# Optimization experiments

Measured on AMD Instinct MI355X. Metric: run time of the kernel, lower is better.

Reference implementation:

```python
import jax, jax.numpy as jnp
import numpy as np

N_NODES = 50000
N_EDGES = 800000
IN_CH, HID, LAT = 256, 128, 64


def setup_inputs() -> dict:
    key = jax.random.key(0)
    k1, k2, k3, k4 = jax.random.split(key, 4)
    x = jax.random.normal(k1, (N_NODES, IN_CH), dtype=jnp.float32)
    edge_index = jax.random.randint(k2, (2, N_EDGES), 0, N_NODES, dtype=jnp.int64)
    W1 = jax.random.normal(k3, (IN_CH, HID), dtype=jnp.float32) * (1.0 / np.sqrt(IN_CH))
    b1 = jnp.zeros((HID,), dtype=jnp.float32)
    W2 = jax.random.normal(k4, (HID, LAT), dtype=jnp.float32) * (1.0 / np.sqrt(HID))
    b2 = jnp.zeros((LAT,), dtype=jnp.float32)
    return {"x": x, "edge_index": edge_index, "W1": W1, "b1": b1, "W2": W2, "b2": b2}


def gcn_conv(x, src, dst, deg_inv_sqrt, W, b):
    # PyG GCNConv: h = x @ W; out[dst] += d_dst^-1/2 * d_src^-1/2 * h[src]; + bias
    h = x @ W                                   # [N, out]
    norm = deg_inv_sqrt[src] * deg_inv_sqrt[dst]  # [E+N]
    msg = h[src] * norm[:, None]                # [E+N, out] (gather + scale)
    out = jax.ops.segment_sum(msg, dst, num_segments=x.shape[0])
    return out + b


def reference(x, edge_index, W1, b1, W2, b2):
    n = x.shape[0]
    loop = jnp.arange(n, dtype=edge_index.dtype)
    # add self loops (GCNConv default)
    src = jnp.concatenate([edge_index[0], loop])
    dst = jnp.concatenate([edge_index[1], loop])
    deg = jax.ops.segment_sum(jnp.ones_like(dst, dtype=x.dtype), dst, num_segments=n)
    deg_inv_sqrt = jnp.where(deg > 0, jax.lax.rsqrt(deg), 0.0)
    h = jax.nn.relu(gcn_conv(x, src, dst, deg_inv_sqrt, W1, b1))
    h = jax.nn.relu(gcn_conv(h, src, dst, deg_inv_sqrt, W2, b2))
    return h
```

## Files before the change

kernel.cpp:

```cpp
#include <hip/hip_runtime.h>

#define N_NODES 50000
#define N_EDGES 800000
#define IN_CH 256
#define HID 128
#define LAT 64
#define CAP 64
#define NBIN 196
#define BINCAP 4864

typedef __attribute__((ext_vector_type(8))) short short8;
typedef __attribute__((ext_vector_type(16))) float f32x16;

static __device__ __forceinline__ unsigned short bf16_rne(float x) {
    unsigned u = __float_as_uint(x);
    unsigned r = (u + 0x7FFFu + ((u >> 16) & 1u)) >> 16;
    return (unsigned short)r;
}
static __device__ __forceinline__ float bf16_to_f(unsigned short h) {
    return __uint_as_float(((unsigned)h) << 16);
}

static __device__ __forceinline__ void add8(uint4 p, float* a) {
    a[0] += __uint_as_float(p.x << 16);
    a[1] += __uint_as_float(p.x & 0xFFFF0000u);
    a[2] += __uint_as_float(p.y << 16);
    a[3] += __uint_as_float(p.y & 0xFFFF0000u);
    a[4] += __uint_as_float(p.z << 16);
    a[5] += __uint_as_float(p.z & 0xFFFF0000u);
    a[6] += __uint_as_float(p.w << 16);
    a[7] += __uint_as_float(p.w & 0xFFFF0000u);
}
static __device__ __forceinline__ void fma8(uint4 p, float m, float* a) {
    a[0] = fmaf(m, __uint_as_float(p.x << 16), a[0]);
    a[1] = fmaf(m, __uint_as_float(p.x & 0xFFFF0000u), a[1]);
    a[2] = fmaf(m, __uint_as_float(p.y << 16), a[2]);
    a[3] = fmaf(m, __uint_as_float(p.y & 0xFFFF0000u), a[3]);
    a[4] = fmaf(m, __uint_as_float(p.z << 16), a[4]);
    a[5] = fmaf(m, __uint_as_float(p.z & 0xFFFF0000u), a[5]);
    a[6] = fmaf(m, __uint_as_float(p.w << 16), a[6]);
    a[7] = fmaf(m, __uint_as_float(p.w & 0xFFFF0000u), a[7]);
}

template <int K, int NN>
static __device__ __forceinline__ void split_store(const float* __restrict__ W,
                                                   unsigned short* __restrict__ Wf, int i) {
    constexpr int CT = NN / 32;
    int k = i / NN, n = i % NN;
    float w = W[i];
    unsigned short hi = bf16_rne(w);
    unsigned short lo = bf16_rne(w - bf16_to_f(hi));
    size_t off = ((size_t)((k >> 4) * CT + (n >> 5)) * 64 + ((n & 31) + 32 * ((k >> 3) & 1))) * 8 + (k & 7);
    Wf[off] = hi;
    Wf[(size_t)K * NN + off] = lo;
}

__global__ __launch_bounds__(256) void prep_kernel(const float* __restrict__ W1,
                                                   const float* __restrict__ W2,
                                                   int* __restrict__ binCnt,
                                                   unsigned short* __restrict__ W1f,
                                                   unsigned short* __restrict__ W2f) {
    int i = blockIdx.x * blockDim.x + threadIdx.x;
    if (i < NBIN) binCnt[i] = 0;
    if (i < IN_CH * HID) split_store<IN_CH, HID>(W1, W1f, i);
    if (i < HID * LAT) split_store<HID, LAT>(W2, W2f, i);
}

__global__ __launch_bounds__(256) void fill1_kernel(const int* __restrict__ ei,
                                                    int* __restrict__ binCnt,
                                                    unsigned int* __restrict__ binBuf, int E) {
    __shared__ int hist[NBIN];
    __shared__ int base[NBIN];
    const int tid = threadIdx.x;
    for (int i = tid; i < NBIN; i += 256) hist[i] = 0;
    __syncthreads();

    const int e0 = blockIdx.x * 2048 + tid;
    unsigned int pk[8];
    int bn[8], ofs[8];
#pragma unroll
    for (int i = 0; i < 8; ++i) {
        int e = e0 + 256 * i;
        bool v = e < E;
        int s = v ? ei[e] : 0;
        int d = v ? ei[E + e] : 0;
        bn[i] = d >> 8;
        pk[i] = (unsigned int)s | ((unsigned int)(d & 255) << 16);
        ofs[i] = v ? atomicAdd(&hist[bn[i]], 1) : -1;
    }
    __syncthreads();
    for (int i = tid; i < NBIN; i += 256)
        base[i] = hist[i] ? atomicAdd(&binCnt[i], hist[i]) : 0;
    __syncthreads();
#pragma unroll
    for (int i = 0; i < 8; ++i) {
        if (ofs[i] >= 0) {
            int p = base[bn[i]] + ofs[i];
            if (p < BINCAP) binBuf[(size_t)bn[i] * BINCAP + p] = pk[i];
        }
    }
}

__global__ __launch_bounds__(256) void fill2_kernel(const int* __restrict__ binCnt,
                                                    const unsigned int* __restrict__ binBuf,
                                                    int* __restrict__ cnt,
                                                    unsigned short* __restrict__ colb) {
    __shared__ int lcnt[256];
    const int b = blockIdx.x;
    const int tid = threadIdx.x;
    lcnt[tid] = 0;
    __syncthreads();
    int n = binCnt[b]; if (n > BINCAP) n = BINCAP;
    const int node0 = b << 8;
    for (int i = tid; i < n; i += 256) {
        unsigned int pk = binBuf[(size_t)b * BINCAP + i];
        int local = pk >> 16;
        int s = pk & 0xFFFF;
        int slot = atomicAdd(&lcnt[local], 1);
        if (slot < CAP) colb[(size_t)(node0 + local) * CAP + slot] = (unsigned short)s;
    }
    __syncthreads();
    int node = node0 + tid;
    if (node < N_NODES) cnt[node] = lcnt[tid];
}

template <int K, int NN, bool AFP32>
__global__ __launch_bounds__(256) void gemm_kernel(const void* __restrict__ Av,
                                                   const unsigned short* __restrict__ Wf,
                                                   const int* __restrict__ cnt,
                                                   unsigned short* __restrict__ C, int M) {
    constexpr int CT = NN / 32;
    constexpr int MT = (NN == 128) ? 2 : 1;
    __shared__ unsigned short As[8 * 512];
    __shared__ unsigned short Bs[2 * 2 * CT * 512];

    const int tid = threadIdx.x;
    const int lane = tid & 63;
    const int w = tid >> 6;
    const int row0 = blockIdx.x * 128;
    const int rtb = (NN == 128) ? ((w >> 1) * 2) : w;
    const int ctb = (NN == 128) ? ((w & 1) * 2) : 0;

    f32x16 acc[MT][2];
#pragma unroll
    for (int mt = 0; mt < MT; ++mt)
#pragma unroll
        for (int nt = 0; nt < 2; ++nt)
#pragma unroll
            for (int q = 0; q < 16; ++q) acc[mt][nt][q] = 0.0f;

    for (int kt = 0; kt < K; kt += 32) {
        if constexpr (AFP32) {
            const float* A = (const float*)Av;
#pragma unroll
            for (int i = 0; i < 4; ++i) {
                int f = tid + 256 * i;
                int m = f >> 3, kq = f & 7;
                int row = row0 + m; if (row >= M) row = M - 1;
                const float4 v = *(const float4*)(A + (size_t)row * K + kt + kq * 4);
                ushort4 hi4 = make_ushort4(bf16_rne(v.x), bf16_rne(v.y), bf16_rne(v.z), bf16_rne(v.w));
                int k0 = kq * 4;
                int s = k0 >> 4, half = (k0 >> 3) & 1, j0 = k0 & 7, t = m >> 5;
                int ln = (m & 31) + 32 * half;
                *(ushort4*)&As[((s * 4 + t) << 9) + (ln << 3) + j0] = hi4;
            }
        } else {
            const unsigned short* A = (const unsigned short*)Av;
#pragma unroll
            for (int i = 0; i < 2; ++i) {
                int f = tid + 256 * i;
                int m = f >> 2, kc = f & 3;
                int row = row0 + m; if (row >= M) row = M - 1;
                uint4 v = *(const uint4*)(A + (size_t)row * K + kt + kc * 8);
                int s = kc >> 1, half = kc & 1, t = m >> 5;
                int ln = (m & 31) + 32 * half;
                *(uint4*)&As[((s * 4 + t) << 9) + (ln << 3)] = v;
            }
        }
        {
            const int sg0 = kt >> 4;
#pragma unroll
            for (int p = 0; p < 2; ++p)
#pragma unroll
                for (int sl = 0; sl < 2; ++sl) {
                    const float4* src = (const float4*)(Wf + (size_t)p * K * NN + (size_t)(sg0 + sl) * CT * 512);
                    float4* dst = (float4*)(Bs + (((p * 2 + sl) * CT) << 9));
                    for (int c0 = w * 64; c0 < CT * 64; c0 += 256) {
                        __builtin_amdgcn_global_load_lds(
                            (const __attribute__((address_space(1))) unsigned int*)(src + c0 + lane),
                            (__attribute__((address_space(3))) unsigned int*)(dst + c0),
                            16, 0, 0);
                    }
                }
        }
        __syncthreads();

#pragma unroll
        for (int sl = 0; sl < 2; ++sl) {
            short8 a[MT], bh[2], bl[2];
#pragma unroll
            for (int mt = 0; mt < MT; ++mt)
                a[mt] = *(const short8*)&As[((sl * 4 + rtb + mt) << 9) + (lane << 3)];
#pragma unroll
            for (int nt = 0; nt < 2; ++nt) {
                bh[nt] = *(const short8*)&Bs[((sl * CT + ctb + nt) << 9) + (lane << 3)];
                bl[nt] = *(const short8*)&Bs[(((2 + sl) * CT + ctb + nt) << 9) + (lane << 3)];
            }
#pragma unroll
            for (int mt = 0; mt < MT; ++mt)
#pragma unroll
                for (int nt = 0; nt < 2; ++nt) {
                    acc[mt][nt] = __builtin_amdgcn_mfma_f32_32x32x16_bf16(a[mt], bh[nt], acc[mt][nt], 0, 0, 0);
                    acc[mt][nt] = __builtin_amdgcn_mfma_f32_32x32x16_bf16(a[mt], bl[nt], acc[mt][nt], 0, 0, 0);
                }
        }
        __syncthreads();
    }

#pragma unroll
    for (int mt = 0; mt < MT; ++mt) {
#pragma unroll
        for (int r = 0; r < 16; ++r) {
            int rowl = (rtb + mt) * 32 + (r & 3) + 8 * (r >> 2) + 4 * (lane >> 5);
            int row = row0 + rowl;
            if (row < M) {
                float sc = rsqrtf((float)cnt[row] + 1.0f);
#pragma unroll
                for (int nt = 0; nt < 2; ++nt) {
                    int col = (ctb + nt) * 32 + (lane & 31);
                    C[(size_t)row * NN + col] = bf16_rne(acc[mt][nt][r] * sc);
                }
            }
        }
    }
}

template <int C, bool OBF16>
__global__ __launch_bounds__(256) void agg_kernel(const int* __restrict__ cnt,
                                                  const unsigned short* __restrict__ colb,
                                                  const unsigned short* __restrict__ hs,
                                                  const float* __restrict__ bias,
                                                  void* __restrict__ outv, int N) {
    constexpr int LPN = C / 8;
    constexpr int NPW = 64 / LPN;
    int node = (int)((blockIdx.x * blockDim.x + threadIdx.x) >> 6);
    int lane = threadIdx.x & 63;
    if (node >= N) return;
    const int g = lane / LPN;
    const int c = lane % LPN;

    int deg = cnt[node];
    int kk = deg < CAP ? deg : CAP;

    float acc[8];
#pragma unroll
    for (int q = 0; q < 8; ++q) acc[q] = 0.0f;
    if (g == 0) add8(*(const uint4*)(hs + (size_t)node * C + c * 8), acc);

    int myc = (lane < kk) ? (int)colb[(size_t)node * CAP + lane] : 0;

    int j = 0;
    for (; j + NPW * 4 <= kk; j += NPW * 4) {
        int s0 = __shfl(myc, j + g);
        int s1 = __shfl(myc, j + g + NPW);
        int s2 = __shfl(myc, j + g + 2 * NPW);
        int s3 = __shfl(myc, j + g + 3 * NPW);
        uint4 p0 = *(const uint4*)(hs + (size_t)s0 * C + c * 8);
        uint4 p1 = *(const uint4*)(hs + (size_t)s1 * C + c * 8);
        uint4 p2 = *(const uint4*)(hs + (size_t)s2 * C + c * 8);
        uint4 p3 = *(const uint4*)(hs + (size_t)s3 * C + c * 8);
        add8(p0, acc); add8(p1, acc); add8(p2, acc); add8(p3, acc);
    }
    if (j < kk) {
        bool v0 = (j + g) < kk, v1 = (j + g + NPW) < kk,
             v2 = (j + g + 2 * NPW) < kk, v3 = (j + g + 3 * NPW) < kk;
        int s0 = __shfl(myc, v0 ? (j + g) : 0);
        int s1 = __shfl(myc, v1 ? (j + g + NPW) : 0);
        int s2 = __shfl(myc, v2 ? (j + g + 2 * NPW) : 0);
        int s3 = __shfl(myc, v3 ? (j + g + 3 * NPW) : 0);
        uint4 p0 = *(const uint4*)(hs + (size_t)s0 * C + c * 8);
        uint4 p1 = *(const uint4*)(hs + (size_t)s1 * C + c * 8);
        uint4 p2 = *(const uint4*)(hs + (size_t)s2 * C + c * 8);
        uint4 p3 = *(const uint4*)(hs + (size_t)s3 * C + c * 8);
        fma8(p0, v0 ? 1.0f : 0.0f, acc);
        fma8(p1, v1 ? 1.0f : 0.0f, acc);
        fma8(p2, v2 ? 1.0f : 0.0f, acc);
        fma8(p3, v3 ? 1.0f : 0.0f, acc);
    }

#pragma unroll
    for (int s = LPN; s < 64; s <<= 1)
#pragma unroll
        for (int q = 0; q < 8; ++q) acc[q] += __shfl_xor(acc[q], s);

    if (lane < LPN) {
        float di = rsqrtf((float)deg + 1.0f);
        float o[8];
#pragma unroll
        for (int q = 0; q < 8; ++q)
            o[q] = fmaxf(fmaf(di, acc[q], bias[c * 8 + q]), 0.0f);
        if constexpr (OBF16) {
            unsigned short* out = (unsigned short*)outv;
            ushort4 lo4 = make_ushort4(bf16_rne(o[0]), bf16_rne(o[1]), bf16_rne(o[2]), bf16_rne(o[3]));
            ushort4 hi4 = make_ushort4(bf16_rne(o[4]), bf16_rne(o[5]), bf16_rne(o[6]), bf16_rne(o[7]));
            *(ushort4*)(out + (size_t)node * C + c * 8) = lo4;
            *(ushort4*)(out + (size_t)node * C + c * 8 + 4) = hi4;
        } else {
            float* out = (float*)outv;
            float4 o0 = {o[0], o[1], o[2], o[3]};
            float4 o1 = {o[4], o[5], o[6], o[7]};
            *(float4*)(out + (size_t)node * C + c * 8) = o0;
            *(float4*)(out + (size_t)node * C + c * 8 + 4) = o1;
        }
    }
}

extern "C" void kernel_launch(void* const* d_in, const int* in_sizes, int n_in,
                              void* d_out, int out_size, void* d_ws, size_t ws_size,
                              hipStream_t stream) {
    const float* x  = (const float*)d_in[0];
    const int*   ei = (const int*)d_in[1];
    const float* W1 = (const float*)d_in[2];
    const float* b1 = (const float*)d_in[3];
    const float* W2 = (const float*)d_in[4];
    const float* b2 = (const float*)d_in[5];

    const int N = N_NODES, E = N_EDGES;

    char* ws = (char*)d_ws;
    size_t off = 0;
    auto alloc = [&](size_t bytes) {
        void* p = ws + off;
        off = (off + bytes + 255) & ~(size_t)255;
        return p;
    };
    int*            cnt    = (int*)alloc((size_t)N * 4);
    unsigned short* colb   = (unsigned short*)alloc((size_t)N * CAP * 2);
    int*            binCnt = (int*)alloc((size_t)NBIN * 4);
    unsigned int*   binBuf = (unsigned int*)alloc((size_t)NBIN * BINCAP * 4);
    unsigned short* W1f    = (unsigned short*)alloc((size_t)2 * IN_CH * HID * 2);
    unsigned short* W2f    = (unsigned short*)alloc((size_t)2 * HID * LAT * 2);
    unsigned short* h1s    = (unsigned short*)alloc((size_t)N * HID * 2);
    unsigned short* act1   = (unsigned short*)alloc((size_t)N * HID * 2);
    unsigned short* h2s    = h1s;

    prep_kernel<<<(N + 255) / 256, 256, 0, stream>>>(W1, W2, binCnt, W1f, W2f);
    fill1_kernel<<<(E + 2047) / 2048, 256, 0, stream>>>(ei, binCnt, binBuf, E);
    fill2_kernel<<<NBIN, 256, 0, stream>>>(binCnt, binBuf, cnt, colb);

    gemm_kernel<IN_CH, HID, true><<<(N + 127) / 128, 256, 0, stream>>>(x, W1f, cnt, h1s, N);
    agg_kernel<HID, true><<<(N + 3) / 4, 256, 0, stream>>>(cnt, colb, h1s, b1, act1, N);

    gemm_kernel<HID, LAT, false><<<(N + 127) / 128, 256, 0, stream>>>(act1, W2f, cnt, h2s, N);
    agg_kernel<LAT, false><<<(N + 3) / 4, 256, 0, stream>>>(cnt, colb, h2s, b2, d_out, N);
}
```

Before: 213.6 us.

## Halve GEMM row tile to 64 and stage weights via plain vector loads

```diff
diff --git a/kernel.cpp b/kernel.cpp
--- a/kernel.cpp
+++ b/kernel.cpp
@@ -130,106 +130,85 @@
                                                    const int* __restrict__ cnt,
                                                    unsigned short* __restrict__ C, int M) {
     constexpr int CT = NN / 32;
-    constexpr int MT = (NN == 128) ? 2 : 1;
-    __shared__ unsigned short As[8 * 512];
+    constexpr int NT = (NN == 128) ? 2 : 1;
+    __shared__ unsigned short As[4 * 512];
     __shared__ unsigned short Bs[2 * 2 * CT * 512];
 
     const int tid = threadIdx.x;
     const int lane = tid & 63;
     const int w = tid >> 6;
-    const int row0 = blockIdx.x * 128;
-    const int rtb = (NN == 128) ? ((w >> 1) * 2) : w;
-    const int ctb = (NN == 128) ? ((w & 1) * 2) : 0;
-
-    f32x16 acc[MT][2];
-#pragma unroll
-    for (int mt = 0; mt < MT; ++mt)
-#pragma unroll
-        for (int nt = 0; nt < 2; ++nt)
-#pragma unroll
-            for (int q = 0; q < 16; ++q) acc[mt][nt][q] = 0.0f;
+    const int row0 = blockIdx.x * 64;
+    const int rt = w >> 1;
+    const int ct0 = (NN == 128) ? ((w & 1) * 2) : (w & 1);
+
+    f32x16 acc[NT];
+#pragma unroll
+    for (int nt = 0; nt < NT; ++nt)
+#pragma unroll
+        for (int q = 0; q < 16; ++q) acc[nt][q] = 0.0f;
 
     for (int kt = 0; kt < K; kt += 32) {
-        if constexpr (AFP32) {
-            const float* A = (const float*)Av;
-#pragma unroll
-            for (int i = 0; i < 4; ++i) {
-                int f = tid + 256 * i;
-                int m = f >> 3, kq = f & 7;
-                int row = row0 + m; if (row >= M) row = M - 1;
-                const float4 v = *(const float4*)(A + (size_t)row * K + kt + kq * 4);
-                ushort4 hi4 = make_ushort4(bf16_rne(v.x), bf16_rne(v.y), bf16_rne(v.z), bf16_rne(v.w));
-                int k0 = kq * 4;
-                int s = k0 >> 4, half = (k0 >> 3) & 1, j0 = k0 & 7, t = m >> 5;
-                int ln = (m & 31) + 32 * half;
-                *(ushort4*)&As[((s * 4 + t) << 9) + (ln << 3) + j0] = hi4;
-            }
-        } else {
-            const unsigned short* A = (const unsigned short*)Av;
-#pragma unroll
-            for (int i = 0; i < 2; ++i) {
-                int f = tid + 256 * i;
-                int m = f >> 2, kc = f & 3;
-                int row = row0 + m; if (row >= M) row = M - 1;
-                uint4 v = *(const uint4*)(A + (size_t)row * K + kt + kc * 8);
-                int s = kc >> 1, half = kc & 1, t = m >> 5;
-                int ln = (m & 31) + 32 * half;
-                *(uint4*)&As[((s * 4 + t) << 9) + (ln << 3)] = v;
-            }
+        {
+            int m = tid >> 2, kc = tid & 3;
+            int row = row0 + m; if (row >= M) row = M - 1;
+            int s = kc >> 1, half = kc & 1, t = m >> 5;
+            int ln = (m & 31) + 32 * half;
+            uint4 v;
+            if constexpr (AFP32) {
+                const float* A = (const float*)Av;
+                const float4 v0 = *(const float4*)(A + (size_t)row * K + kt + kc * 8);
+                const float4 v1 = *(const float4*)(A + (size_t)row * K + kt + kc * 8 + 4);
+                v.x = (unsigned)bf16_rne(v0.x) | ((unsigned)bf16_rne(v0.y) << 16);
+                v.y = (unsigned)bf16_rne(v0.z) | ((unsigned)bf16_rne(v0.w) << 16);
+                v.z = (unsigned)bf16_rne(v1.x) | ((unsigned)bf16_rne(v1.y) << 16);
+                v.w = (unsigned)bf16_rne(v1.z) | ((unsigned)bf16_rne(v1.w) << 16);
+            } else {
+                const unsigned short* A = (const unsigned short*)Av;
+                v = *(const uint4*)(A + (size_t)row * K + kt + kc * 8);
+            }
+            *(uint4*)&As[((s * 2 + t) << 9) + (ln << 3)] = v;
         }
         {
             const int sg0 = kt >> 4;
 #pragma unroll
-            for (int p = 0; p < 2; ++p)
-#pragma unroll
-                for (int sl = 0; sl < 2; ++sl) {
-                    const float4* src = (const float4*)(Wf + (size_t)p * K * NN + (size_t)(sg0 + sl) * CT * 512);
-                    float4* dst = (float4*)(Bs + (((p * 2 + sl) * CT) << 9));
-                    for (int c0 = w * 64; c0 < CT * 64; c0 += 256) {
-                        __builtin_amdgcn_global_load_lds(
-                            (const __attribute__((address_space(1))) unsigned int*)(src + c0 + lane),
-                            (__attribute__((address_space(3))) unsigned int*)(dst + c0),
-                            16, 0, 0);
-                    }
-                }
+            for (int i0 = 0; i0 < CT * 256; i0 += 256) {
+                int i = i0 + tid;
+                int psl = i / (CT * 64), rem = i % (CT * 64);
+                int p = psl >> 1, sl = psl & 1;
+                const uint4* src = (const uint4*)(Wf + (size_t)p * K * NN + (size_t)(sg0 + sl) * CT * 512);
+                ((uint4*)Bs)[i] = src[rem];
+            }
         }
         __syncthreads();
 
 #pragma unroll
         for (int sl = 0; sl < 2; ++sl) {
-            short8 a[MT], bh[2], bl[2];
-#pragma unroll
-            for (int mt = 0; mt < MT; ++mt)
-                a[mt] = *(const short8*)&As[((sl * 4 + rtb + mt) << 9) + (lane << 3)];
-#pragma unroll
-            for (int nt = 0; nt < 2; ++nt) {
-                bh[nt] = *(const short8*)&Bs[((sl * CT + ctb + nt) << 9) + (lane << 3)];
-                bl[nt] = *(const short8*)&Bs[(((2 + sl) * CT + ctb + nt) << 9) + (lane << 3)];
-            }
-#pragma unroll
-            for (int mt = 0; mt < MT; ++mt)
-#pragma unroll
-                for (int nt = 0; nt < 2; ++nt) {
-                    acc[mt][nt] = __builtin_amdgcn_mfma_f32_32x32x16_bf16(a[mt], bh[nt], acc[mt][nt], 0, 0, 0);
-                    acc[mt][nt] = __builtin_amdgcn_mfma_f32_32x32x16_bf16(a[mt], bl[nt], acc[mt][nt], 0, 0, 0);
-                }
+            short8 a = *(const short8*)&As[((sl * 2 + rt) << 9) + (lane << 3)];
+            short8 bh[NT], bl[NT];
+#pragma unroll
+            for (int nt = 0; nt < NT; ++nt) {
+                bh[nt] = *(const short8*)&Bs[((sl * CT + ct0 + nt) << 9) + (lane << 3)];
+                bl[nt] = *(const short8*)&Bs[(((2 + sl) * CT + ct0 + nt) << 9) + (lane << 3)];
+            }
+#pragma unroll
+            for (int nt = 0; nt < NT; ++nt) {
+                acc[nt] = __builtin_amdgcn_mfma_f32_32x32x16_bf16(a, bh[nt], acc[nt], 0, 0, 0);
+                acc[nt] = __builtin_amdgcn_mfma_f32_32x32x16_bf16(a, bl[nt], acc[nt], 0, 0, 0);
+            }
         }
         __syncthreads();
     }
 
 #pragma unroll
-    for (int mt = 0; mt < MT; ++mt) {
-#pragma unroll
-        for (int r = 0; r < 16; ++r) {
-            int rowl = (rtb + mt) * 32 + (r & 3) + 8 * (r >> 2) + 4 * (lane >> 5);
-            int row = row0 + rowl;
-            if (row < M) {
-                float sc = rsqrtf((float)cnt[row] + 1.0f);
-#pragma unroll
-                for (int nt = 0; nt < 2; ++nt) {
-                    int col = (ctb + nt) * 32 + (lane & 31);
-                    C[(size_t)row * NN + col] = bf16_rne(acc[mt][nt][r] * sc);
-                }
+    for (int r = 0; r < 16; ++r) {
+        int rowl = rt * 32 + (r & 3) + 8 * (r >> 2) + 4 * (lane >> 5);
+        int row = row0 + rowl;
+        if (row < M) {
+            float sc = rsqrtf((float)cnt[row] + 1.0f);
+#pragma unroll
+            for (int nt = 0; nt < NT; ++nt) {
+                int col = (ct0 + nt) * 32 + (lane & 31);
+                C[(size_t)row * NN + col] = bf16_rne(acc[nt][r] * sc);
             }
         }
     }
@@ -348,9 +327,9 @@
     fill1_kernel<<<(E + 2047) / 2048, 256, 0, stream>>>(ei, binCnt, binBuf, E);
     fill2_kernel<<<NBIN, 256, 0, stream>>>(binCnt, binBuf, cnt, colb);
 
-    gemm_kernel<IN_CH, HID, true><<<(N + 127) / 128, 256, 0, stream>>>(x, W1f, cnt, h1s, N);
+    gemm_kernel<IN_CH, HID, true><<<(N + 63) / 64, 256, 0, stream>>>(x, W1f, cnt, h1s, N);
     agg_kernel<HID, true><<<(N + 3) / 4, 256, 0, stream>>>(cnt, colb, h1s, b1, act1, N);
 
-    gemm_kernel<HID, LAT, false><<<(N + 127) / 128, 256, 0, stream>>>(act1, W2f, cnt, h2s, N);
+    gemm_kernel<HID, LAT, false><<<(N + 63) / 64, 256, 0, stream>>>(act1, W2f, cnt, h2s, N);
     agg_kernel<LAT, false><<<(N + 3) / 4, 256, 0, stream>>>(cnt, colb, h2s, b2, d_out, N);
 }
```

Result: faster. 198.3 us (-7.2%).
